# Kernel optimization log

Measured on AMD Instinct MI355X. Metric: run time of the kernel, lower is better.

Reference implementation:

```python
import jax, jax.numpy as jnp
import numpy as np

N_NODES = 100000
N_EDGES = 3200000
NFEAT, NHID, NCLASS = 256, 128, 16


def setup_inputs() -> dict:
    key = jax.random.key(0)
    ks = jax.random.split(key, 7)
    features = jax.random.normal(ks[0], (N_NODES, NFEAT), dtype=jnp.float32)
    edge_index = jax.random.randint(ks[1], (2, N_EDGES), 0, N_NODES, dtype=jnp.int32)
    edge_weight = jax.random.uniform(ks[2], (N_EDGES,), dtype=jnp.float32)
    s1 = 1.0 / np.sqrt(NFEAT)
    s2 = 1.0 / np.sqrt(NHID)
    W1 = jax.random.uniform(ks[3], (NFEAT, NHID), dtype=jnp.float32, minval=-s1, maxval=s1)
    b1 = jax.random.uniform(ks[4], (NHID,), dtype=jnp.float32, minval=-s1, maxval=s1)
    W2 = jax.random.uniform(ks[5], (NHID, NCLASS), dtype=jnp.float32, minval=-s2, maxval=s2)
    b2 = jax.random.uniform(ks[6], (NCLASS,), dtype=jnp.float32, minval=-s2, maxval=s2)
    return {"features": features, "edge_index": edge_index, "edge_weight": edge_weight,
            "W1": W1, "b1": b1, "W2": W2, "b2": b2}


def _sgconv(x, edge_index, edge_weight, W, b, num_nodes):
    # gcn_norm with self-loops (PyG default for SGConv, K=1)
    row, col = edge_index[0], edge_index[1]
    loop = jnp.arange(num_nodes, dtype=row.dtype)
    row = jnp.concatenate([row, loop])
    col = jnp.concatenate([col, loop])
    ew = jnp.concatenate([edge_weight, jnp.ones((num_nodes,), edge_weight.dtype)])
    deg = jax.ops.segment_sum(ew, col, num_segments=num_nodes)
    dinv = jnp.where(deg > 0, jax.lax.rsqrt(deg), 0.0)
    norm = dinv[row] * ew * dinv[col]                       # [E+N]
    msg = x[row] * norm[:, None]                            # gather + scale
    out = jax.ops.segment_sum(msg, col, num_segments=num_nodes)  # scatter-add to targets
    return out @ W + b


def reference(features, edge_index, edge_weight, W1, b1, W2, b2):
    n = features.shape[0]
    h = jax.nn.relu(_sgconv(features, edge_index, edge_weight, W1, b1, n))
    # dropout is identity in eval mode (training=False)
    h = _sgconv(h, edge_index, edge_weight, W2, b2, n)
    return jax.nn.log_softmax(h, axis=1)
```

## Files before the change

### kernel.cpp

```cpp
#include <hip/hip_runtime.h>
#include <hip/hip_bf16.h>

typedef unsigned short u16;
typedef unsigned char u8;
typedef short bf16x8 __attribute__((ext_vector_type(8)));
typedef float f32x4 __attribute__((ext_vector_type(4)));
typedef float f32x2 __attribute__((ext_vector_type(2)));

__device__ __forceinline__ float blo(unsigned u) { return __uint_as_float(u << 16); }
__device__ __forceinline__ float bhi(unsigned u) { return __uint_as_float(u & 0xFFFF0000u); }
__device__ __forceinline__ u16 f2bf(float f) {
    unsigned x = __float_as_uint(f);
    x += 0x7fffu + ((x >> 16) & 1u);
    return (u16)(x >> 16);
}
__device__ __forceinline__ u8 f2fp8(float f) {
    return (u8)(__builtin_amdgcn_cvt_pk_fp8_f32(f, f, 0, false) & 0xFF);
}

#define CAP 80
#define NB_SHIFT 7
#define BNODES 128
#define CAPB 4608
#define MAXNB 800
#define PK 136
#define EPB 4096


__global__ __launch_bounds__(256) void k_prepw(const float* __restrict__ W1, u16* __restrict__ W1t) {
    int t = blockIdx.x * 256 + threadIdx.x;
    int k = t >> 5;
    int n4 = (t & 31) * 4;
    float4 v = *(const float4*)(W1 + k * 128 + n4);
    W1t[(n4 + 0) * 256 + k] = f2bf(v.x);
    W1t[(n4 + 1) * 256 + k] = f2bf(v.y);
    W1t[(n4 + 2) * 256 + k] = f2bf(v.z);
    W1t[(n4 + 3) * 256 + k] = f2bf(v.w);
}


__global__ __launch_bounds__(512) void k_bin(const int* __restrict__ row, const int* __restrict__ col,
                                             const float* __restrict__ ew, int* __restrict__ gcount,
                                             int2* __restrict__ binned, int E, int NB) {
    __shared__ int cl[MAXNB];
    int t = threadIdx.x;
    int base = blockIdx.x * EPB;
    for (int i = t; i < NB; i += 512) cl[i] = 0;
    __syncthreads();

    int e0 = base + t * 8;
    bool full = (e0 + 8 <= E);
    int cs[8];
    if (full) {
        int4 c0 = *(const int4*)(col + e0);
        int4 c1 = *(const int4*)(col + e0 + 4);
        cs[0] = c0.x; cs[1] = c0.y; cs[2] = c0.z; cs[3] = c0.w;
        cs[4] = c1.x; cs[5] = c1.y; cs[6] = c1.z; cs[7] = c1.w;
#pragma unroll
        for (int j = 0; j < 8; ++j) atomicAdd(&cl[cs[j] >> NB_SHIFT], 1);
    } else {
#pragma unroll
        for (int j = 0; j < 8; ++j) {
            int e = e0 + j;
            cs[j] = (e < E) ? col[e] : 0;
            if (e < E) atomicAdd(&cl[cs[j] >> NB_SHIFT], 1);
        }
    }
    __syncthreads();

    for (int b = t; b < NB; b += 512) {
        int c = cl[b];
        cl[b] = (c > 0) ? atomicAdd(gcount + b, c) : 0;
    }
    __syncthreads();

    if (full) {
        int4 r0 = *(const int4*)(row + e0);
        int4 r1 = *(const int4*)(row + e0 + 4);
        float4 w0 = *(const float4*)(ew + e0);
        float4 w1 = *(const float4*)(ew + e0 + 4);
        int rs[8] = {r0.x, r0.y, r0.z, r0.w, r1.x, r1.y, r1.z, r1.w};
        float wv[8] = {w0.x, w0.y, w0.z, w0.w, w1.x, w1.y, w1.z, w1.w};
#pragma unroll
        for (int j = 0; j < 8; ++j) {
            int c = cs[j];
            int b = c >> NB_SHIFT;
            int slot = atomicAdd(&cl[b], 1);
            if (slot < CAPB)
                binned[(size_t)b * CAPB + slot] =
                    make_int2(rs[j] | ((c & (BNODES - 1)) << 20), __float_as_int(wv[j]));
        }
    } else {
#pragma unroll
        for (int j = 0; j < 8; ++j) {
            int e = e0 + j;
            if (e < E) {
                int c = cs[j];
                int b = c >> NB_SHIFT;
                int slot = atomicAdd(&cl[b], 1);
                if (slot < CAPB)
                    binned[(size_t)b * CAPB + slot] =
                        make_int2(row[e] | ((c & (BNODES - 1)) << 20), __float_as_int(ew[e]));
            }
        }
    }
}


__global__ __launch_bounds__(512) void k_fill(const int* __restrict__ gcount, const int2* __restrict__ binned,
                                              int* __restrict__ cnt, float* __restrict__ dinv,
                                              int2* __restrict__ ell, int N, int NB) {
    __shared__ int   c128[BNODES];
    __shared__ float d128[BNODES];
    int t = threadIdx.x;
    int b = blockIdx.x;
    if (t < BNODES) { c128[t] = 0; d128[t] = 0.f; }
    __syncthreads();
    int M = min(gcount[b], CAPB);
    int nb0 = b << NB_SHIFT;
    const int2* src = binned + (size_t)b * CAPB;
    for (int j = t; j < M; j += 512) {
        int2 rec = src[j];
        int r  = rec.x & 0xFFFFF;
        int lc = rec.x >> 20;
        int slot = atomicAdd(&c128[lc], 1);
        if (slot < CAP) ell[(size_t)(nb0 + lc) * CAP + slot] = make_int2(r, rec.y);
        atomicAdd(&d128[lc], __int_as_float(rec.y));
    }
    __syncthreads();
    if (t < BNODES) {
        int n = nb0 + t;
        if (n < N) {
            cnt[n]  = c128[t];
            dinv[n] = rsqrtf(1.0f + d128[t]);
        }
    }
}


__global__ __launch_bounds__(256) void k_gemm1(const float* __restrict__ feat, const u16* __restrict__ W1t,
                                               const float* __restrict__ dinv, u8* __restrict__ h0f, int N) {
    __shared__ u16 As[64 * PK];
    __shared__ u16 Bs[128 * PK];
    int t = threadIdx.x;
    int nb0 = blockIdx.x * 64;
    int wv = t >> 6, lane = t & 63;
    int m16 = lane & 15, quad = lane >> 4;

    f32x4 zero4 = {0.f, 0.f, 0.f, 0.f};
    f32x4 acc[8];
#pragma unroll
    for (int i = 0; i < 8; ++i) acc[i] = zero4;

    for (int half = 0; half < 2; ++half) {
        int k0 = half * 128;
#pragma unroll
        for (int i = 0; i < 8; ++i) {
            int idx = t + 256 * i;
            int r = idx >> 5;
            int c4 = idx & 31;
            int gn = nb0 + r;
            float4 v = (gn < N) ? *(const float4*)(feat + (size_t)gn * 256 + k0 + c4 * 4)
                                : make_float4(0.f, 0.f, 0.f, 0.f);
            ushort4 o;
            o.x = f2bf(v.x); o.y = f2bf(v.y); o.z = f2bf(v.z); o.w = f2bf(v.w);
            *(ushort4*)(As + r * PK + c4 * 4) = o;
        }
#pragma unroll
        for (int i = 0; i < 8; ++i) {
            int idx = t + 256 * i;
            int r = idx >> 4;
            int c = (idx & 15) * 8;
            *(uint4*)(Bs + r * PK + c) = *(const uint4*)(W1t + r * 256 + k0 + c);
        }
        __syncthreads();
        const u16* arow = As + (wv * 16 + m16) * PK + quad * 8;
        const u16* brow = Bs + m16 * PK + quad * 8;
#pragma unroll
        for (int kc = 0; kc < 4; ++kc) {
            bf16x8 a = *(const bf16x8*)(arow + kc * 32);
#pragma unroll
            for (int tn = 0; tn < 8; ++tn) {
                bf16x8 b = *(const bf16x8*)(brow + tn * 16 * PK + kc * 32);
                acc[tn] = __builtin_amdgcn_mfma_f32_16x16x32_bf16(a, b, acc[tn], 0, 0, 0);
            }
        }
        __syncthreads();
    }
    int node0 = nb0 + wv * 16 + quad * 4;
    float dv[4];
#pragma unroll
    for (int r = 0; r < 4; ++r) dv[r] = (node0 + r < N) ? dinv[node0 + r] : 0.f;
#pragma unroll
    for (int tn = 0; tn < 8; ++tn) {
        int hid = tn * 16 + m16;
#pragma unroll
        for (int r = 0; r < 4; ++r) {
            int gn = node0 + r;
            if (gn < N) h0f[(size_t)gn * 128 + hid] = f2fp8(acc[tn][r] * dv[r]);
        }
    }
}


__global__ __launch_bounds__(256) void k_agg1(const u8* __restrict__ h0f, const float* __restrict__ dinv,
                                              const int* __restrict__ cnt, const int2* __restrict__ ell,
                                              const float* __restrict__ b1, const float* __restrict__ W2,
                                              u16* __restrict__ h2b, int N) {
    __shared__ float s_row[16][132];
    __shared__ float s_w2[2048];
    int t = threadIdx.x;
    int wv = t >> 6, lane = t & 63;
    int g = lane >> 4;
    int fl = lane & 15;
    int f = fl * 8;
    int ln = wv * 4 + g;
    int n = blockIdx.x * 16 + ln;
    bool active = n < N;

    {
        float4 wa = *(const float4*)(W2 + t * 8);
        float4 wb = *(const float4*)(W2 + t * 8 + 4);
        *(float4*)&s_w2[t * 8]     = wa;
        *(float4*)&s_w2[t * 8 + 4] = wb;
    }

    float acc[8];
#pragma unroll
    for (int j = 0; j < 8; ++j) acc[j] = 0.f;

#define ACC8(V, W)                                                              \
    {                                                                           \
        f32x2 p0 = __builtin_amdgcn_cvt_pk_f32_fp8((V).x, false);               \
        f32x2 p1 = __builtin_amdgcn_cvt_pk_f32_fp8((V).x, true);                \
        f32x2 p2 = __builtin_amdgcn_cvt_pk_f32_fp8((V).y, false);               \
        f32x2 p3 = __builtin_amdgcn_cvt_pk_f32_fp8((V).y, true);                \
        acc[0] += p0[0] * (W); acc[1] += p0[1] * (W);                           \
        acc[2] += p1[0] * (W); acc[3] += p1[1] * (W);                           \
        acc[4] += p2[0] * (W); acc[5] += p2[1] * (W);                           \
        acc[6] += p3[0] * (W); acc[7] += p3[1] * (W);                           \
    }

    if (active) {
        float dn = dinv[n];
        {
            uint2 sv = *(const uint2*)(h0f + (size_t)n * 128 + f);
            ACC8(sv, dn);
        }
        int m = min(cnt[n], CAP);
        const int2* ep = ell + (size_t)n * CAP;
        int k = 0;
        for (; k + 3 < m; k += 4) {
            int2 e0 = ep[k], e1 = ep[k + 1], e2 = ep[k + 2], e3 = ep[k + 3];
            uint2 v0 = *(const uint2*)(h0f + (size_t)e0.x * 128 + f);
            uint2 v1 = *(const uint2*)(h0f + (size_t)e1.x * 128 + f);
            uint2 v2 = *(const uint2*)(h0f + (size_t)e2.x * 128 + f);
            uint2 v3 = *(const uint2*)(h0f + (size_t)e3.x * 128 + f);
            float w0 = __int_as_float(e0.y) * dn;
            float w1 = __int_as_float(e1.y) * dn;
            float w2 = __int_as_float(e2.y) * dn;
            float w3 = __int_as_float(e3.y) * dn;
            ACC8(v0, w0);
            ACC8(v1, w1);
            ACC8(v2, w2);
            ACC8(v3, w3);
        }
        for (; k < m; ++k) {
            int2 e = ep[k];
            float w = __int_as_float(e.y) * dn;
            uint2 v = *(const uint2*)(h0f + (size_t)e.x * 128 + f);
            ACC8(v, w);
        }
        float4 bA = *(const float4*)(b1 + f);
        float4 bB = *(const float4*)(b1 + f + 4);
        float4 oA, oB;
        oA.x = fmaxf(acc[0] + bA.x, 0.f); oA.y = fmaxf(acc[1] + bA.y, 0.f);
        oA.z = fmaxf(acc[2] + bA.z, 0.f); oA.w = fmaxf(acc[3] + bA.w, 0.f);
        oB.x = fmaxf(acc[4] + bB.x, 0.f); oB.y = fmaxf(acc[5] + bB.y, 0.f);
        oB.z = fmaxf(acc[6] + bB.z, 0.f); oB.w = fmaxf(acc[7] + bB.w, 0.f);
        *(float4*)&s_row[ln][f]     = oA;
        *(float4*)&s_row[ln][f + 4] = oB;
    }
#undef ACC8
    __syncthreads();

    int nn = t >> 4;
    int c = t & 15;
    int gn = blockIdx.x * 16 + nn;
    float a2 = 0.f;
#pragma unroll
    for (int k = 0; k < 128; ++k) a2 += s_row[nn][k] * s_w2[k * 16 + c];
    if (gn < N) h2b[(size_t)gn * 16 + c] = f2bf(a2 * dinv[gn]);
}


__global__ __launch_bounds__(256) void k_agg2(const u16* __restrict__ g2b, const float* __restrict__ dinv,
                                              const int* __restrict__ cnt, const int2* __restrict__ ell,
                                              const float* __restrict__ b2, float* __restrict__ out, int N) {
    int t = threadIdx.x;
    int wv = t >> 6, lane = t & 63;
    int g = lane >> 3;
    int fl = lane & 7;
    int n = blockIdx.x * 32 + wv * 8 + g;
    if (n >= N) return;
    float dn = dinv[n];
    float2 acc;
    {
        unsigned sv = *(const unsigned*)(g2b + (size_t)n * 16 + fl * 2);
        acc.x = blo(sv) * dn;
        acc.y = bhi(sv) * dn;
    }
    int m = min(cnt[n], CAP);
    const int2* ep = ell + (size_t)n * CAP;
    int k = 0;
    for (; k + 3 < m; k += 4) {
        int2 e0 = ep[k], e1 = ep[k + 1], e2 = ep[k + 2], e3 = ep[k + 3];
        unsigned v0 = *(const unsigned*)(g2b + (size_t)e0.x * 16 + fl * 2);
        unsigned v1 = *(const unsigned*)(g2b + (size_t)e1.x * 16 + fl * 2);
        unsigned v2 = *(const unsigned*)(g2b + (size_t)e2.x * 16 + fl * 2);
        unsigned v3 = *(const unsigned*)(g2b + (size_t)e3.x * 16 + fl * 2);
        float w0 = __int_as_float(e0.y) * dn;
        float w1 = __int_as_float(e1.y) * dn;
        float w2 = __int_as_float(e2.y) * dn;
        float w3 = __int_as_float(e3.y) * dn;
        acc.x += blo(v0) * w0 + blo(v1) * w1 + blo(v2) * w2 + blo(v3) * w3;
        acc.y += bhi(v0) * w0 + bhi(v1) * w1 + bhi(v2) * w2 + bhi(v3) * w3;
    }
    for (; k < m; ++k) {
        int2 e = ep[k];
        float w = __int_as_float(e.y) * dn;
        unsigned v = *(const unsigned*)(g2b + (size_t)e.x * 16 + fl * 2);
        acc.x += blo(v) * w;
        acc.y += bhi(v) * w;
    }
    float v0 = acc.x + b2[fl * 2];
    float v1 = acc.y + b2[fl * 2 + 1];
    float mx = fmaxf(v0, v1);
    mx = fmaxf(mx, __shfl_xor(mx, 1));
    mx = fmaxf(mx, __shfl_xor(mx, 2));
    mx = fmaxf(mx, __shfl_xor(mx, 4));
    float ex = __expf(v0 - mx) + __expf(v1 - mx);
    ex += __shfl_xor(ex, 1);
    ex += __shfl_xor(ex, 2);
    ex += __shfl_xor(ex, 4);
    float lse = mx + __logf(ex);
    *(float2*)(out + (size_t)n * 16 + fl * 2) = make_float2(v0 - lse, v1 - lse);
}


extern "C" void kernel_launch(void* const* d_in, const int* in_sizes, int n_in,
                              void* d_out, int out_size, void* d_ws, size_t ws_size,
                              hipStream_t stream) {
    const float* feat = (const float*)d_in[0];
    const int*   eidx = (const int*)d_in[1];
    const float* ew   = (const float*)d_in[2];
    const float* W1   = (const float*)d_in[3];
    const float* b1   = (const float*)d_in[4];
    const float* W2   = (const float*)d_in[5];
    const float* b2   = (const float*)d_in[6];
    float* out = (float*)d_out;

    int N = in_sizes[0] / 256;
    int E = in_sizes[2];
    const int* row = eidx;
    const int* col = eidx + E;
    int NB = (N + BNODES - 1) >> NB_SHIFT;

    char* ws = (char*)d_ws;
    size_t off = 0;
    auto take = [&](size_t bytes) { void* p = ws + off; off += (bytes + 255) & ~(size_t)255; return p; };
    int*   cnt    = (int*)take((size_t)N * 4);
    float* dinv   = (float*)take((size_t)N * 4);
    int*   gcount = (int*)take((size_t)NB * 4);
    u16*   W1t    = (u16*)take((size_t)128 * 256 * 2);
    int2*  ell    = (int2*)take((size_t)N * CAP * 8);
    size_t ubytes = (size_t)NB * CAPB * 8;
    size_t h0fb   = (size_t)N * 128;
    void*  uni    = take(ubytes > h0fb ? ubytes : h0fb);
    u16*   h2b    = (u16*)take((size_t)N * 16 * 2);
    int2*  binned = (int2*)uni;
    u8*    h0f    = (u8*)uni;

    auto cdiv = [](long long a, long long b) { return (int)((a + b - 1) / b); };

    hipMemsetAsync(gcount, 0, (size_t)NB * 4, stream);
    k_bin   <<<cdiv(E, EPB), 512, 0, stream>>>(row, col, ew, gcount, binned, E, NB);
    k_fill  <<<NB, 512, 0, stream>>>(gcount, binned, cnt, dinv, ell, N, NB);
    k_prepw <<<32, 256, 0, stream>>>(W1, W1t);

    k_gemm1 <<<cdiv(N, 64), 256, 0, stream>>>(feat, W1t, dinv, h0f, N);
    k_agg1  <<<cdiv(N, 16), 256, 0, stream>>>(h0f, dinv, cnt, ell, b1, W2, h2b, N);
    k_agg2  <<<cdiv(N, 32), 256, 0, stream>>>(h2b, dinv, cnt, ell, b2, out, N);
}
```

Before: 398.4 us.

## Widen agg1 per-lane gathers to 16 bytes and process 32 nodes per block

The first aggregation kernel now assigns 8 lanes per node, each loading 16 fp8 features (uint4) instead of 8, so one block of 256 threads covers 32 nodes. Edge pairs are read as int4, and accumulation uses packed f32x2 multiply-adds. The fused W2 projection also computes two output columns per thread with a packed bf16 store. The aim is fewer, wider memory transactions and fewer blocks. The cost is more registers per thread and twice the LDS for the row buffer.

```diff
diff --git a/kernel.cpp b/kernel.cpp
--- a/kernel.cpp
+++ b/kernel.cpp
@@ -207,15 +207,15 @@
                                               const int* __restrict__ cnt, const int2* __restrict__ ell,
                                               const float* __restrict__ b1, const float* __restrict__ W2,
                                               u16* __restrict__ h2b, int N) {
-    __shared__ float s_row[16][132];
+    __shared__ float s_row[32][132];
     __shared__ float s_w2[2048];
     int t = threadIdx.x;
     int wv = t >> 6, lane = t & 63;
-    int g = lane >> 4;
-    int fl = lane & 15;
-    int f = fl * 8;
-    int ln = wv * 4 + g;
-    int n = blockIdx.x * 16 + ln;
+    int g = lane >> 3;
+    int fl = lane & 7;
+    int f = fl * 16;
+    int ln = wv * 8 + g;
+    int n = blockIdx.x * 32 + ln;
     bool active = n < N;
 
     {
@@ -225,72 +225,84 @@
         *(float4*)&s_w2[t * 8 + 4] = wb;
     }
 
-    float acc[8];
-#pragma unroll
-    for (int j = 0; j < 8; ++j) acc[j] = 0.f;
-
-#define ACC8(V, W)                                                              \
-    {                                                                           \
-        f32x2 p0 = __builtin_amdgcn_cvt_pk_f32_fp8((V).x, false);               \
-        f32x2 p1 = __builtin_amdgcn_cvt_pk_f32_fp8((V).x, true);                \
-        f32x2 p2 = __builtin_amdgcn_cvt_pk_f32_fp8((V).y, false);               \
-        f32x2 p3 = __builtin_amdgcn_cvt_pk_f32_fp8((V).y, true);                \
-        acc[0] += p0[0] * (W); acc[1] += p0[1] * (W);                           \
-        acc[2] += p1[0] * (W); acc[3] += p1[1] * (W);                           \
-        acc[4] += p2[0] * (W); acc[5] += p2[1] * (W);                           \
-        acc[6] += p3[0] * (W); acc[7] += p3[1] * (W);                           \
+    f32x2 acc2[8];
+#pragma unroll
+    for (int j = 0; j < 8; ++j) acc2[j] = (f32x2){0.f, 0.f};
+
+#define ACC16(V, W)                                                                  \
+    {                                                                                \
+        f32x2 w2 = {(W), (W)};                                                       \
+        acc2[0] += __builtin_amdgcn_cvt_pk_f32_fp8((V).x, false) * w2;               \
+        acc2[1] += __builtin_amdgcn_cvt_pk_f32_fp8((V).x, true)  * w2;               \
+        acc2[2] += __builtin_amdgcn_cvt_pk_f32_fp8((V).y, false) * w2;               \
+        acc2[3] += __builtin_amdgcn_cvt_pk_f32_fp8((V).y, true)  * w2;               \
+        acc2[4] += __builtin_amdgcn_cvt_pk_f32_fp8((V).z, false) * w2;               \
+        acc2[5] += __builtin_amdgcn_cvt_pk_f32_fp8((V).z, true)  * w2;               \
+        acc2[6] += __builtin_amdgcn_cvt_pk_f32_fp8((V).w, false) * w2;               \
+        acc2[7] += __builtin_amdgcn_cvt_pk_f32_fp8((V).w, true)  * w2;               \
     }
 
     if (active) {
         float dn = dinv[n];
         {
-            uint2 sv = *(const uint2*)(h0f + (size_t)n * 128 + f);
-            ACC8(sv, dn);
+            uint4 sv = *(const uint4*)(h0f + (size_t)n * 128 + f);
+            ACC16(sv, dn);
         }
         int m = min(cnt[n], CAP);
         const int2* ep = ell + (size_t)n * CAP;
         int k = 0;
         for (; k + 3 < m; k += 4) {
-            int2 e0 = ep[k], e1 = ep[k + 1], e2 = ep[k + 2], e3 = ep[k + 3];
-            uint2 v0 = *(const uint2*)(h0f + (size_t)e0.x * 128 + f);
-            uint2 v1 = *(const uint2*)(h0f + (size_t)e1.x * 128 + f);
-            uint2 v2 = *(const uint2*)(h0f + (size_t)e2.x * 128 + f);
-            uint2 v3 = *(const uint2*)(h0f + (size_t)e3.x * 128 + f);
-            float w0 = __int_as_float(e0.y) * dn;
-            float w1 = __int_as_float(e1.y) * dn;
-            float w2 = __int_as_float(e2.y) * dn;
-            float w3 = __int_as_float(e3.y) * dn;
-            ACC8(v0, w0);
-            ACC8(v1, w1);
-            ACC8(v2, w2);
-            ACC8(v3, w3);
+            int4 e01 = *(const int4*)(ep + k);
+            int4 e23 = *(const int4*)(ep + k + 2);
+            uint4 v0 = *(const uint4*)(h0f + (size_t)e01.x * 128 + f);
+            uint4 v1 = *(const uint4*)(h0f + (size_t)e01.z * 128 + f);
+            uint4 v2 = *(const uint4*)(h0f + (size_t)e23.x * 128 + f);
+            uint4 v3 = *(const uint4*)(h0f + (size_t)e23.z * 128 + f);
+            float w0 = __int_as_float(e01.y) * dn;
+            float w1 = __int_as_float(e01.w) * dn;
+            float w2x = __int_as_float(e23.y) * dn;
+            float w3 = __int_as_float(e23.w) * dn;
+            ACC16(v0, w0);
+            ACC16(v1, w1);
+            ACC16(v2, w2x);
+            ACC16(v3, w3);
         }
         for (; k < m; ++k) {
             int2 e = ep[k];
             float w = __int_as_float(e.y) * dn;
-            uint2 v = *(const uint2*)(h0f + (size_t)e.x * 128 + f);
-            ACC8(v, w);
-        }
-        float4 bA = *(const float4*)(b1 + f);
-        float4 bB = *(const float4*)(b1 + f + 4);
-        float4 oA, oB;
-        oA.x = fmaxf(acc[0] + bA.x, 0.f); oA.y = fmaxf(acc[1] + bA.y, 0.f);
-        oA.z = fmaxf(acc[2] + bA.z, 0.f); oA.w = fmaxf(acc[3] + bA.w, 0.f);
-        oB.x = fmaxf(acc[4] + bB.x, 0.f); oB.y = fmaxf(acc[5] + bB.y, 0.f);
-        oB.z = fmaxf(acc[6] + bB.z, 0.f); oB.w = fmaxf(acc[7] + bB.w, 0.f);
-        *(float4*)&s_row[ln][f]     = oA;
-        *(float4*)&s_row[ln][f + 4] = oB;
-    }
-#undef ACC8
-    __syncthreads();
-
-    int nn = t >> 4;
-    int c = t & 15;
-    int gn = blockIdx.x * 16 + nn;
-    float a2 = 0.f;
-#pragma unroll
-    for (int k = 0; k < 128; ++k) a2 += s_row[nn][k] * s_w2[k * 16 + c];
-    if (gn < N) h2b[(size_t)gn * 16 + c] = f2bf(a2 * dinv[gn]);
+            uint4 v = *(const uint4*)(h0f + (size_t)e.x * 128 + f);
+            ACC16(v, w);
+        }
+#undef ACC16
+#pragma unroll
+        for (int q = 0; q < 4; ++q) {
+            float4 bq = *(const float4*)(b1 + f + q * 4);
+            float4 o;
+            o.x = fmaxf(acc2[q * 2 + 0][0] + bq.x, 0.f);
+            o.y = fmaxf(acc2[q * 2 + 0][1] + bq.y, 0.f);
+            o.z = fmaxf(acc2[q * 2 + 1][0] + bq.z, 0.f);
+            o.w = fmaxf(acc2[q * 2 + 1][1] + bq.w, 0.f);
+            *(float4*)&s_row[ln][f + q * 4] = o;
+        }
+    }
+    __syncthreads();
+
+    int nn = t >> 3;
+    int c2 = (t & 7) * 2;
+    int gn = blockIdx.x * 32 + nn;
+    f32x2 a2 = {0.f, 0.f};
+#pragma unroll
+    for (int k = 0; k < 128; ++k) {
+        f32x2 wv2 = *(const f32x2*)&s_w2[k * 16 + c2];
+        float r = s_row[nn][k];
+        f32x2 r2 = {r, r};
+        a2 += r2 * wv2;
+    }
+    if (gn < N) {
+        float dg = dinv[gn];
+        unsigned pk = ((unsigned)f2bf(a2[1] * dg) << 16) | (unsigned)f2bf(a2[0] * dg);
+        *(unsigned*)(h2b + (size_t)gn * 16 + c2) = pk;
+    }
 }
 
 
@@ -389,6 +401,6 @@
     k_prepw <<<32, 256, 0, stream>>>(W1, W1t);
 
     k_gemm1 <<<cdiv(N, 64), 256, 0, stream>>>(feat, W1t, dinv, h0f, N);
-    k_agg1  <<<cdiv(N, 16), 256, 0, stream>>>(h0f, dinv, cnt, ell, b1, W2, h2b, N);
+    k_agg1  <<<cdiv(N, 32), 256, 0, stream>>>(h0f, dinv, cnt, ell, b1, W2, h2b, N);
     k_agg2  <<<cdiv(N, 32), 256, 0, stream>>>(h2b, dinv, cnt, ell, b2, out, N);
 }
```

Result: no change. 398.6 us (+0.1%).
